# Kernel optimization log

Hardware: AMD Instinct MI355X
Metric: run time of the kernel (lower is better)

Reference implementation:

```python
import jax, jax.numpy as jnp
import numpy as np

B, S, D, H = 2, 2048, 1024, 16
DK = D // H


def setup_inputs() -> dict:
    key = jax.random.key(0)
    ks = jax.random.split(key, 12)
    scale = 1.0 / np.sqrt(D)
    inp = {
        "Q": jax.random.normal(ks[0], (B, S, D), jnp.float32),
        "K": jax.random.normal(ks[1], (B, S, D), jnp.float32),
        "V": jax.random.normal(ks[2], (B, S, D), jnp.float32),
        # causal mask, broadcastable to [B, H, S, S]; 0 -> masked
        "Mask": jnp.tril(jnp.ones((S, S), jnp.int32))[None, None],
        "Wq": jax.random.normal(ks[3], (D, D), jnp.float32) * scale,
        "bq": jnp.zeros((D,), jnp.float32),
        "Wk": jax.random.normal(ks[4], (D, D), jnp.float32) * scale,
        "bk": jnp.zeros((D,), jnp.float32),
        "Wv": jax.random.normal(ks[5], (D, D), jnp.float32) * scale,
        "bv": jnp.zeros((D,), jnp.float32),
        "Wo": jax.random.normal(ks[6], (D, D), jnp.float32) * scale,
        "bo": jnp.zeros((D,), jnp.float32),
    }
    return inp


def _heads(x):
    # [B, S, D] -> [B, H, S, DK]
    return x.reshape(B, S, H, DK).transpose(0, 2, 1, 3)


def reference(Q, K, V, Mask, Wq, bq, Wk, bk, Wv, bv, Wo, bo):
    q = _heads(Q @ Wq.T + bq)
    k = _heads(K @ Wk.T + bk)
    v = _heads(V @ Wv.T + bv)
    # NOTE: original module does NOT scale by 1/sqrt(d_k)
    logits = jnp.einsum("bhqd,bhkd->bhqk", q, k)
    logits = jnp.where(Mask == 0, jnp.float32(-1e9), logits)
    attn = jax.nn.softmax(logits, axis=-1)  # dropout p=0.0 -> identity
    ctx = jnp.einsum("bhqk,bhkd->bhqd", attn, v)
    ctx = ctx.transpose(0, 2, 1, 3).reshape(B, S, D)
    return ctx @ Wo.T + bo
```

## Files before the change

kernel.cpp:

```cpp
#include <hip/hip_runtime.h>
#include <hip/hip_bf16.h>

#define B_  2
#define S_  2048
#define D_  1024
#define H_  16
#define DK_ 64
#define M_  (B_ * S_)

typedef __bf16 bf16;
typedef __bf16 bf16x8 __attribute__((ext_vector_type(8)));
typedef __bf16 bf16x4 __attribute__((ext_vector_type(4)));
typedef float  f32x4  __attribute__((ext_vector_type(4)));

#define MFMA16(a, b, c) __builtin_amdgcn_mfma_f32_16x16x32_bf16((a), (b), (c), 0, 0, 0)

__device__ __forceinline__ void gl2lds16(const bf16* g, bf16* l) {
    __builtin_amdgcn_global_load_lds((const __attribute__((address_space(1))) void*)g,
                                     (__attribute__((address_space(3))) void*)l, 16, 0, 0);
}

struct CastArgs { const float* src[7]; bf16* dst[7]; };

__global__ __launch_bounds__(256) void cast_all(CastArgs a) {
    int i = blockIdx.x * 256 + threadIdx.x;
    int seg, off;
    if (i < 3145728) { seg = i >> 20; off = i & 1048575; }
    else { int j = i - 3145728; seg = 3 + (j >> 18); off = j & 262143; }
    float4 v = ((const float4*)a.src[seg])[off];
    bf16x4 o;
    o[0] = (bf16)v.x; o[1] = (bf16)v.y; o[2] = (bf16)v.z; o[3] = (bf16)v.w;
    *(bf16x4*)&a.dst[seg][(size_t)off * 4] = o;
}

struct QkvArgs { const bf16* A[3]; const bf16* W[3]; const float* bias[3]; bf16* out[3]; };

__global__ __launch_bounds__(256, 3) void gemm_qkv(QkvArgs ar) {
    __shared__ char smem[34816];
    bf16* As = (bf16*)smem;
    bf16* Bs = (bf16*)(smem + 16384);
    bf16* Cs = (bf16*)smem;

    const int z = blockIdx.z;
    const bf16* A  = ar.A[z];
    const bf16* Bt = ar.W[z];
    const float* bias = ar.bias[z];
    bf16* Out = ar.out[z];
    const int mode = (z == 2) ? 1 : 0;

    const int t = threadIdx.x, lane = t & 63, w = t >> 6;
    const int lr = lane & 15, lq = lane >> 4;
    const int wm = (w >> 1) * 64, wn = (w & 1) * 64;
    const int n0 = blockIdx.x * 128, m0 = blockIdx.y * 128;

    const bf16* Ag[4]; const bf16* Bg[4]; bf16* Al[4]; bf16* Bl[4];
#pragma unroll
    for (int i = 0; i < 4; ++i) {
        int c = i * 256 + w * 64 + lane;
        int row = c >> 3, x = (c & 7) ^ (row & 7);
        Ag[i] = A  + (size_t)(m0 + row) * 1024 + x * 8;
        Bg[i] = Bt + (size_t)(n0 + row) * 1024 + x * 8;
        Al[i] = As + (i * 256 + w * 64) * 8;
        Bl[i] = Bs + (i * 256 + w * 64) * 8;
    }

    f32x4 acc[4][4];
#pragma unroll
    for (int mi = 0; mi < 4; ++mi)
#pragma unroll
        for (int ni = 0; ni < 4; ++ni) acc[mi][ni] = 0.0f;

    for (int k0 = 0; k0 < 1024; k0 += 64) {
        __syncthreads();
#pragma unroll
        for (int i = 0; i < 4; ++i) {
            gl2lds16(Ag[i] + k0, Al[i]);
            gl2lds16(Bg[i] + k0, Bl[i]);
        }
        __syncthreads();
#pragma unroll
        for (int ks = 0; ks < 2; ++ks) {
            bf16x8 af[4], bfr[4];
#pragma unroll
            for (int mi = 0; mi < 4; ++mi) {
                int row = wm + mi * 16 + lr;
                af[mi] = *(const bf16x8*)&As[row * 64 + ((ks * 4 + lq) ^ (row & 7)) * 8];
            }
#pragma unroll
            for (int ni = 0; ni < 4; ++ni) {
                int row = wn + ni * 16 + lr;
                bfr[ni] = *(const bf16x8*)&Bs[row * 64 + ((ks * 4 + lq) ^ (row & 7)) * 8];
            }
#pragma unroll
            for (int mi = 0; mi < 4; ++mi)
#pragma unroll
                for (int ni = 0; ni < 4; ++ni) acc[mi][ni] = MFMA16(af[mi], bfr[ni], acc[mi][ni]);
        }
    }

    if (mode == 0) {
#pragma unroll
        for (int mi = 0; mi < 4; ++mi) {
#pragma unroll
            for (int ni = 0; ni < 4; ++ni) {
                int gn = n0 + wn + ni * 16 + lr;
                float bv = bias[gn];
#pragma unroll
                for (int r = 0; r < 4; ++r) {
                    int gm = m0 + wm + mi * 16 + lq * 4 + r;
                    float v = acc[mi][ni][r] + bv;
                    int b = gm >> 11, s = gm & (S_ - 1);
                    int h = gn >> 6, dk = gn & 63;
                    Out[(((size_t)(b * H_ + h) * S_ + s) << 6) + dk] = (bf16)v;
                }
            }
        }
    } else {
        __syncthreads();
#pragma unroll
        for (int mi = 0; mi < 4; ++mi) {
#pragma unroll
            for (int ni = 0; ni < 4; ++ni) {
                int n = wn + ni * 16 + lr;
                float bv = bias[n0 + n];
                bf16x4 pk;
#pragma unroll
                for (int r = 0; r < 4; ++r) pk[r] = (bf16)(acc[mi][ni][r] + bv);
                *(bf16x4*)&Cs[n * 136 + wm + mi * 16 + lq * 4] = pk;
            }
        }
        __syncthreads();
        const int b = m0 >> 11, s0 = m0 & (S_ - 1);
#pragma unroll
        for (int j = 0; j < 8; ++j) {
            int cc = j * 256 + t;
            int n = cc >> 4, cm = cc & 15;
            int gn = n0 + n, h = gn >> 6, dk = gn & 63;
            bf16x8 v = *(const bf16x8*)&Cs[n * 136 + cm * 8];
            *(bf16x8*)&Out[(((size_t)(b * H_ + h) * DK_ + dk) << 11) + s0 + cm * 8] = v;
        }
    }
}

__global__ __launch_bounds__(256, 2) void gemm_out(const bf16* __restrict__ A,
                                                   const bf16* __restrict__ Bt,
                                                   const float* __restrict__ bias,
                                                   float* __restrict__ Out) {
    __shared__ bf16 As[64 * 64];
    __shared__ bf16 Bs[128 * 64];

    const int t = threadIdx.x, lane = t & 63, w = t >> 6;
    const int lr = lane & 15, lq = lane >> 4;
    const int wm = (w >> 1) * 32, wn = (w & 1) * 64;
    const int n0 = blockIdx.x * 128, m0 = blockIdx.y * 64;

    const bf16* Ag[2]; bf16* Al[2];
#pragma unroll
    for (int i = 0; i < 2; ++i) {
        int c = i * 256 + w * 64 + lane;
        int row = c >> 3, x = (c & 7) ^ (row & 7);
        Ag[i] = A + (size_t)(m0 + row) * 1024 + x * 8;
        Al[i] = As + (i * 256 + w * 64) * 8;
    }
    const bf16* Bg[4]; bf16* Bl[4];
#pragma unroll
    for (int i = 0; i < 4; ++i) {
        int c = i * 256 + w * 64 + lane;
        int row = c >> 3, x = (c & 7) ^ (row & 7);
        Bg[i] = Bt + (size_t)(n0 + row) * 1024 + x * 8;
        Bl[i] = Bs + (i * 256 + w * 64) * 8;
    }

    f32x4 acc[2][4];
#pragma unroll
    for (int mi = 0; mi < 2; ++mi)
#pragma unroll
        for (int ni = 0; ni < 4; ++ni) acc[mi][ni] = 0.0f;

    for (int k0 = 0; k0 < 1024; k0 += 64) {
        __syncthreads();
#pragma unroll
        for (int i = 0; i < 2; ++i) gl2lds16(Ag[i] + k0, Al[i]);
#pragma unroll
        for (int i = 0; i < 4; ++i) gl2lds16(Bg[i] + k0, Bl[i]);
        __syncthreads();
#pragma unroll
        for (int ks = 0; ks < 2; ++ks) {
            bf16x8 af[2], bfr[4];
#pragma unroll
            for (int mi = 0; mi < 2; ++mi) {
                int row = wm + mi * 16 + lr;
                af[mi] = *(const bf16x8*)&As[row * 64 + ((ks * 4 + lq) ^ (row & 7)) * 8];
            }
#pragma unroll
            for (int ni = 0; ni < 4; ++ni) {
                int row = wn + ni * 16 + lr;
                bfr[ni] = *(const bf16x8*)&Bs[row * 64 + ((ks * 4 + lq) ^ (row & 7)) * 8];
            }
#pragma unroll
            for (int mi = 0; mi < 2; ++mi)
#pragma unroll
                for (int ni = 0; ni < 4; ++ni) acc[mi][ni] = MFMA16(af[mi], bfr[ni], acc[mi][ni]);
        }
    }

#pragma unroll
    for (int mi = 0; mi < 2; ++mi) {
#pragma unroll
        for (int ni = 0; ni < 4; ++ni) {
            int gn = n0 + wn + ni * 16 + lr;
            float bv = bias[gn];
#pragma unroll
            for (int r = 0; r < 4; ++r) {
                int gm = m0 + wm + mi * 16 + lq * 4 + r;
                Out[(size_t)gm * 1024 + gn] = acc[mi][ni][r] + bv;
            }
        }
    }
}

__global__ __launch_bounds__(256, 2) void flash_attn(const bf16* __restrict__ qh,
                                                     const bf16* __restrict__ kh,
                                                     const bf16* __restrict__ vt,
                                                     bf16* __restrict__ ctx) {
    __shared__ char smem[40960];
    bf16* Qs = (bf16*)smem;
    bf16* Ks = (bf16*)(smem + 8192);
    bf16* Ps = (bf16*)(smem + 24576);

    const int id = blockIdx.x;
    const int xcd = id & 7, loc = id >> 3;
    const int bh = xcd * 4 + (loc & 3);
    const int pair = loc >> 2;
    const int b = bh >> 4, h = bh & 15;

    const bf16* Qp = qh + (size_t)bh * S_ * DK_;
    const bf16* Kp = kh + (size_t)bh * S_ * DK_;
    const bf16* Vp = vt + (size_t)bh * DK_ * S_;

    const int t = threadIdx.x, lane = t & 63, w = t >> 6;
    const int lr = lane & 15, lq = lane >> 4;
    const int wq = w & 1, wk = w >> 1;
    bf16* Pw = Ps + w * 2048;

    for (int half = 0; half < 2; ++half) {
        const int qt = half ? (31 - pair) : pair;

#pragma unroll
        for (int i = 0; i < 2; ++i) {
            int c = w * 128 + i * 64 + lane;
            int qrow = c >> 3, xx = (c & 7) ^ (qrow & 7);
            gl2lds16(Qp + (size_t)(qt * 64 + qrow) * 64 + xx * 8, Qs + (w * 128 + i * 64) * 8);
        }

        f32x4 oacc[2][4];
#pragma unroll
        for (int mt = 0; mt < 2; ++mt)
#pragma unroll
            for (int nt = 0; nt < 4; ++nt) oacc[mt][nt] = 0.0f;
        float lpart[2] = {0.f, 0.f};

        const int nkt = qt / 2 + 1;
        for (int kt = 0; kt < nkt; ++kt) {
            __syncthreads();
#pragma unroll
            for (int i = 0; i < 4; ++i) {
                int c = w * 256 + i * 64 + lane;
                int krow = c >> 3, xx = (c & 7) ^ (krow & 7);
                gl2lds16(Kp + (size_t)(kt * 128 + krow) * 64 + xx * 8, Ks + (w * 256 + i * 64) * 8);
            }
            __syncthreads();

            const int k64 = kt * 2 + wk;
            if (k64 <= qt) {
                bf16x8 bv[2][4];
#pragma unroll
                for (int kk = 0; kk < 2; ++kk)
#pragma unroll
                    for (int nt = 0; nt < 4; ++nt)
                        bv[kk][nt] = *(const bf16x8*)(Vp + (size_t)(nt * 16 + lr) * S_ +
                                                      kt * 128 + wk * 64 + kk * 32 + lq * 8);
                f32x4 s[4][2];
#pragma unroll
                for (int mt = 0; mt < 4; ++mt)
#pragma unroll
                    for (int nt = 0; nt < 2; ++nt) s[mt][nt] = 0.0f;
#pragma unroll
                for (int ks = 0; ks < 2; ++ks) {
                    bf16x8 af[4], qf[2];
                    int xx = (ks * 4 + lq) ^ (lr & 7);
#pragma unroll
                    for (int mt = 0; mt < 4; ++mt)
                        af[mt] = *(const bf16x8*)&Ks[(wk * 64 + mt * 16 + lr) * 64 + xx * 8];
#pragma unroll
                    for (int nt = 0; nt < 2; ++nt)
                        qf[nt] = *(const bf16x8*)&Qs[(wq * 32 + nt * 16 + lr) * 64 + xx * 8];
#pragma unroll
                    for (int mt = 0; mt < 4; ++mt)
#pragma unroll
                        for (int nt = 0; nt < 2; ++nt) s[mt][nt] = MFMA16(af[mt], qf[nt], s[mt][nt]);
                }
                const bool diag = (k64 == qt);
#pragma unroll
                for (int mt = 0; mt < 4; ++mt)
#pragma unroll
                    for (int nt = 0; nt < 2; ++nt) {
                        bf16x4 pb;
#pragma unroll
                        for (int r = 0; r < 4; ++r) {
                            int kl = mt * 16 + lq * 4 + r;
                            int qlT = wq * 32 + nt * 16 + lr;
                            float p = (!diag || kl <= qlT) ? __expf(s[mt][nt][r]) : 0.0f;
                            bf16 p16 = (bf16)p;
                            lpart[nt] += (float)p16;
                            pb[r] = p16;
                        }
                        int xx = (2 * mt + (lq >> 1)) ^ (lr & 7);
                        *(bf16x4*)&Pw[(nt * 16 + lr) * 64 + xx * 8 + (lq & 1) * 4] = pb;
                    }
#pragma unroll
                for (int kk = 0; kk < 2; ++kk) {
                    bf16x8 ap[2];
                    int xx = (kk * 4 + lq) ^ (lr & 7);
#pragma unroll
                    for (int mt2 = 0; mt2 < 2; ++mt2)
                        ap[mt2] = *(const bf16x8*)&Pw[(mt2 * 16 + lr) * 64 + xx * 8];
#pragma unroll
                    for (int mt2 = 0; mt2 < 2; ++mt2)
#pragma unroll
                        for (int nt = 0; nt < 4; ++nt)
                            oacc[mt2][nt] = MFMA16(ap[mt2], bv[kk][nt], oacc[mt2][nt]);
                }
            }
        }

        __syncthreads();
#pragma unroll
        for (int nt = 0; nt < 2; ++nt) {
            lpart[nt] += __shfl_xor(lpart[nt], 16);
            lpart[nt] += __shfl_xor(lpart[nt], 32);
        }
        float* Op = (float*)(smem + 24576);
        float* Lh = (float*)smem;
        if (lq == 0)
#pragma unroll
            for (int nt = 0; nt < 2; ++nt) Lh[wk * 64 + wq * 32 + nt * 16 + lr] = lpart[nt];
        if (wk == 1) {
#pragma unroll
            for (int mt = 0; mt < 2; ++mt)
#pragma unroll
                for (int nt = 0; nt < 4; ++nt)
#pragma unroll
                    for (int r = 0; r < 4; ++r) {
                        int row = mt * 16 + lq * 4 + r, col = nt * 16 + lr;
                        int xx = (col >> 2) ^ (row & 15);
                        Op[wq * 2048 + row * 64 + xx * 4 + (col & 3)] = oacc[mt][nt][r];
                    }
        }
        __syncthreads();
        if (wk == 0) {
            float linv[2][4];
#pragma unroll
            for (int mt = 0; mt < 2; ++mt)
#pragma unroll
                for (int r = 0; r < 4; ++r) {
                    int qq = wq * 32 + mt * 16 + lq * 4 + r;
                    linv[mt][r] = 1.0f / (Lh[qq] + Lh[64 + qq]);
                }
#pragma unroll
            for (int mt = 0; mt < 2; ++mt)
#pragma unroll
                for (int nt = 0; nt < 4; ++nt)
#pragma unroll
                    for (int r = 0; r < 4; ++r) {
                        int row = mt * 16 + lq * 4 + r, col = nt * 16 + lr;
                        int xx = (col >> 2) ^ (row & 15);
                        float v = (oacc[mt][nt][r] + Op[wq * 2048 + row * 64 + xx * 4 + (col & 3)]) * linv[mt][r];
                        int q = qt * 64 + wq * 32 + row;
                        ctx[((size_t)(b * S_ + q)) * D_ + h * DK_ + col] = (bf16)v;
                    }
        }
        __syncthreads();
    }
}

extern "C" void kernel_launch(void* const* d_in, const int* in_sizes, int n_in,
                              void* d_out, int out_size, void* d_ws, size_t ws_size,
                              hipStream_t stream) {
    const float* Q  = (const float*)d_in[0];
    const float* K  = (const float*)d_in[1];
    const float* V  = (const float*)d_in[2];
    const float* Wq = (const float*)d_in[4];
    const float* bq = (const float*)d_in[5];
    const float* Wk = (const float*)d_in[6];
    const float* bk = (const float*)d_in[7];
    const float* Wv = (const float*)d_in[8];
    const float* bv = (const float*)d_in[9];
    const float* Wo = (const float*)d_in[10];
    const float* bo = (const float*)d_in[11];

    char* p = (char*)d_ws;
    bf16* Qb  = (bf16*)p;  p += (size_t)M_ * D_ * 2;
    bf16* Kb  = (bf16*)p;  p += (size_t)M_ * D_ * 2;
    bf16* Vb  = (bf16*)p;  p += (size_t)M_ * D_ * 2;
    bf16* Wqb = (bf16*)p;  p += (size_t)D_ * D_ * 2;
    bf16* Wkb = (bf16*)p;  p += (size_t)D_ * D_ * 2;
    bf16* Wvb = (bf16*)p;  p += (size_t)D_ * D_ * 2;
    bf16* Wob = (bf16*)p;  p += (size_t)D_ * D_ * 2;
    bf16* qhd = (bf16*)p;  p += (size_t)M_ * D_ * 2;
    bf16* khd = (bf16*)p;  p += (size_t)M_ * D_ * 2;
    bf16* vtr = (bf16*)p;  p += (size_t)M_ * D_ * 2;
    bf16* ctx = (bf16*)p;  p += (size_t)M_ * D_ * 2;

    CastArgs ca;
    ca.src[0] = Q;  ca.dst[0] = Qb;
    ca.src[1] = K;  ca.dst[1] = Kb;
    ca.src[2] = V;  ca.dst[2] = Vb;
    ca.src[3] = Wq; ca.dst[3] = Wqb;
    ca.src[4] = Wk; ca.dst[4] = Wkb;
    ca.src[5] = Wv; ca.dst[5] = Wvb;
    ca.src[6] = Wo; ca.dst[6] = Wob;
    cast_all<<<16384, 256, 0, stream>>>(ca);

    QkvArgs qa;
    qa.A[0] = Qb;  qa.A[1] = Kb;  qa.A[2] = Vb;
    qa.W[0] = Wqb; qa.W[1] = Wkb; qa.W[2] = Wvb;
    qa.bias[0] = bq; qa.bias[1] = bk; qa.bias[2] = bv;
    qa.out[0] = qhd; qa.out[1] = khd; qa.out[2] = vtr;
    dim3 qgrid(D_ / 128, M_ / 128, 3);
    gemm_qkv<<<qgrid, 256, 0, stream>>>(qa);

    flash_attn<<<512, 256, 0, stream>>>(qhd, khd, vtr, ctx);

    dim3 ogrid(D_ / 128, M_ / 64);
    gemm_out<<<ogrid, 256, 0, stream>>>(ctx, Wob, bo, (float*)d_out);
}
```

Measured before the change: 228.9 us.

## Split flash attention into one q-tile per block, load K/Q directly to registers

The attention kernel now launches one block per 64-row query tile (1024 blocks) instead of pairing a light and a heavy causal tile in one block. The heaviest tiles get the lowest block ids. Q fragments are held in registers, and K fragments are read straight from global memory instead of being staged through LDS with barriers. This cuts LDS use (17KB vs 40KB) and removes the per-iteration syncthreads. In exchange, K tiles are no longer shared through LDS, so each wave re-reads K from global or L2, and the load balance between blocks becomes uneven.

Result: slower. 255.9 us (+11.8%).

```diff
diff --git a/kernel.cpp b/kernel.cpp
--- a/kernel.cpp
+++ b/kernel.cpp
@@ -223,15 +223,15 @@
                                                      const bf16* __restrict__ kh,
                                                      const bf16* __restrict__ vt,
                                                      bf16* __restrict__ ctx) {
-    __shared__ char smem[40960];
-    bf16* Qs = (bf16*)smem;
-    bf16* Ks = (bf16*)(smem + 8192);
-    bf16* Ps = (bf16*)(smem + 24576);
+    __shared__ char smem[17408];
+    float* Lh = (float*)smem;
+    bf16* Ps = (bf16*)(smem + 1024);
+    float* Op = (float*)(smem + 1024);
 
     const int id = blockIdx.x;
     const int xcd = id & 7, loc = id >> 3;
     const int bh = xcd * 4 + (loc & 3);
-    const int pair = loc >> 2;
+    const int qt = 31 - (loc >> 2);
     const int b = bh >> 4, h = bh & 15;
 
     const bf16* Qp = qh + (size_t)bh * S_ * DK_;
@@ -243,144 +243,128 @@
     const int wq = w & 1, wk = w >> 1;
     bf16* Pw = Ps + w * 2048;
 
-    for (int half = 0; half < 2; ++half) {
-        const int qt = half ? (31 - pair) : pair;
-
-#pragma unroll
-        for (int i = 0; i < 2; ++i) {
-            int c = w * 128 + i * 64 + lane;
-            int qrow = c >> 3, xx = (c & 7) ^ (qrow & 7);
-            gl2lds16(Qp + (size_t)(qt * 64 + qrow) * 64 + xx * 8, Qs + (w * 128 + i * 64) * 8);
-        }
-
-        f32x4 oacc[2][4];
+    bf16x8 qreg[2][2];
+#pragma unroll
+    for (int ks = 0; ks < 2; ++ks)
+#pragma unroll
+        for (int nt = 0; nt < 2; ++nt)
+            qreg[ks][nt] = *(const bf16x8*)(Qp +
+                (size_t)(qt * 64 + wq * 32 + nt * 16 + lr) * 64 + ks * 32 + lq * 8);
+
+    f32x4 oacc[2][4];
+#pragma unroll
+    for (int mt = 0; mt < 2; ++mt)
+#pragma unroll
+        for (int nt = 0; nt < 4; ++nt) oacc[mt][nt] = 0.0f;
+    float lpart[2] = {0.f, 0.f};
+
+    const bf16* Kw = Kp + (size_t)(wk * 64 + lr) * 64 + lq * 8;
+    const bf16* Vw = Vp + (size_t)lr * S_ + wk * 64 + lq * 8;
+
+    const int nkt = qt / 2 + 1;
+    for (int kt = 0; kt < nkt; ++kt) {
+        const int k64 = kt * 2 + wk;
+        if (k64 <= qt) {
+            bf16x8 bv[2][4];
+#pragma unroll
+            for (int kk = 0; kk < 2; ++kk)
+#pragma unroll
+                for (int nt = 0; nt < 4; ++nt)
+                    bv[kk][nt] = *(const bf16x8*)(Vw + (size_t)nt * 16 * S_ +
+                                                  kt * 128 + kk * 32);
+            f32x4 s[4][2];
+#pragma unroll
+            for (int mt = 0; mt < 4; ++mt)
+#pragma unroll
+                for (int nt = 0; nt < 2; ++nt) s[mt][nt] = 0.0f;
+#pragma unroll
+            for (int ks = 0; ks < 2; ++ks) {
+                bf16x8 af[4];
+#pragma unroll
+                for (int mt = 0; mt < 4; ++mt)
+                    af[mt] = *(const bf16x8*)(Kw + (size_t)(kt * 128 + mt * 16) * 64 + ks * 32);
+#pragma unroll
+                for (int mt = 0; mt < 4; ++mt)
+#pragma unroll
+                    for (int nt = 0; nt < 2; ++nt) s[mt][nt] = MFMA16(af[mt], qreg[ks][nt], s[mt][nt]);
+            }
+            const bool diag = (k64 == qt);
+#pragma unroll
+            for (int mt = 0; mt < 4; ++mt)
+#pragma unroll
+                for (int nt = 0; nt < 2; ++nt) {
+                    bf16x4 pb;
+#pragma unroll
+                    for (int r = 0; r < 4; ++r) {
+                        int kl = mt * 16 + lq * 4 + r;
+                        int qlT = wq * 32 + nt * 16 + lr;
+                        float p = (!diag || kl <= qlT) ? __expf(s[mt][nt][r]) : 0.0f;
+                        bf16 p16 = (bf16)p;
+                        lpart[nt] += (float)p16;
+                        pb[r] = p16;
+                    }
+                    int xx = (2 * mt + (lq >> 1)) ^ (lr & 7);
+                    *(bf16x4*)&Pw[(nt * 16 + lr) * 64 + xx * 8 + (lq & 1) * 4] = pb;
+                }
+#pragma unroll
+            for (int kk = 0; kk < 2; ++kk) {
+                bf16x8 ap[2];
+                int xx = (kk * 4 + lq) ^ (lr & 7);
+#pragma unroll
+                for (int mt2 = 0; mt2 < 2; ++mt2)
+                    ap[mt2] = *(const bf16x8*)&Pw[(mt2 * 16 + lr) * 64 + xx * 8];
+#pragma unroll
+                for (int mt2 = 0; mt2 < 2; ++mt2)
+#pragma unroll
+                    for (int nt = 0; nt < 4; ++nt)
+                        oacc[mt2][nt] = MFMA16(ap[mt2], bv[kk][nt], oacc[mt2][nt]);
+            }
+        }
+    }
+
+    __syncthreads();
+#pragma unroll
+    for (int nt = 0; nt < 2; ++nt) {
+        lpart[nt] += __shfl_xor(lpart[nt], 16);
+        lpart[nt] += __shfl_xor(lpart[nt], 32);
+    }
+    if (lq == 0)
+#pragma unroll
+        for (int nt = 0; nt < 2; ++nt) Lh[wk * 64 + wq * 32 + nt * 16 + lr] = lpart[nt];
+    if (wk == 1) {
 #pragma unroll
         for (int mt = 0; mt < 2; ++mt)
 #pragma unroll
-            for (int nt = 0; nt < 4; ++nt) oacc[mt][nt] = 0.0f;
-        float lpart[2] = {0.f, 0.f};
-
-        const int nkt = qt / 2 + 1;
-        for (int kt = 0; kt < nkt; ++kt) {
-            __syncthreads();
-#pragma unroll
-            for (int i = 0; i < 4; ++i) {
-                int c = w * 256 + i * 64 + lane;
-                int krow = c >> 3, xx = (c & 7) ^ (krow & 7);
-                gl2lds16(Kp + (size_t)(kt * 128 + krow) * 64 + xx * 8, Ks + (w * 256 + i * 64) * 8);
-            }
-            __syncthreads();
-
-            const int k64 = kt * 2 + wk;
-            if (k64 <= qt) {
-                bf16x8 bv[2][4];
-#pragma unroll
-                for (int kk = 0; kk < 2; ++kk)
-#pragma unroll
-                    for (int nt = 0; nt < 4; ++nt)
-                        bv[kk][nt] = *(const bf16x8*)(Vp + (size_t)(nt * 16 + lr) * S_ +
-                                                      kt * 128 + wk * 64 + kk * 32 + lq * 8);
-                f32x4 s[4][2];
-#pragma unroll
-                for (int mt = 0; mt < 4; ++mt)
-#pragma unroll
-                    for (int nt = 0; nt < 2; ++nt) s[mt][nt] = 0.0f;
-#pragma unroll
-                for (int ks = 0; ks < 2; ++ks) {
-                    bf16x8 af[4], qf[2];
-                    int xx = (ks * 4 + lq) ^ (lr & 7);
-#pragma unroll
-                    for (int mt = 0; mt < 4; ++mt)
-                        af[mt] = *(const bf16x8*)&Ks[(wk * 64 + mt * 16 + lr) * 64 + xx * 8];
-#pragma unroll
-                    for (int nt = 0; nt < 2; ++nt)
-                        qf[nt] = *(const bf16x8*)&Qs[(wq * 32 + nt * 16 + lr) * 64 + xx * 8];
-#pragma unroll
-                    for (int mt = 0; mt < 4; ++mt)
-#pragma unroll
-                        for (int nt = 0; nt < 2; ++nt) s[mt][nt] = MFMA16(af[mt], qf[nt], s[mt][nt]);
+            for (int nt = 0; nt < 4; ++nt)
+#pragma unroll
+                for (int r = 0; r < 4; ++r) {
+                    int row = mt * 16 + lq * 4 + r, col = nt * 16 + lr;
+                    int xx = (col >> 2) ^ (row & 15);
+                    Op[wq * 2048 + row * 64 + xx * 4 + (col & 3)] = oacc[mt][nt][r];
                 }
-                const bool diag = (k64 == qt);
-#pragma unroll
-                for (int mt = 0; mt < 4; ++mt)
-#pragma unroll
-                    for (int nt = 0; nt < 2; ++nt) {
-                        bf16x4 pb;
-#pragma unroll
-                        for (int r = 0; r < 4; ++r) {
-                            int kl = mt * 16 + lq * 4 + r;
-                            int qlT = wq * 32 + nt * 16 + lr;
-                            float p = (!diag || kl <= qlT) ? __expf(s[mt][nt][r]) : 0.0f;
-                            bf16 p16 = (bf16)p;
-                            lpart[nt] += (float)p16;
-                            pb[r] = p16;
-                        }
-                        int xx = (2 * mt + (lq >> 1)) ^ (lr & 7);
-                        *(bf16x4*)&Pw[(nt * 16 + lr) * 64 + xx * 8 + (lq & 1) * 4] = pb;
-                    }
-#pragma unroll
-                for (int kk = 0; kk < 2; ++kk) {
-                    bf16x8 ap[2];
-                    int xx = (kk * 4 + lq) ^ (lr & 7);
-#pragma unroll
-                    for (int mt2 = 0; mt2 < 2; ++mt2)
-                        ap[mt2] = *(const bf16x8*)&Pw[(mt2 * 16 + lr) * 64 + xx * 8];
-#pragma unroll
-                    for (int mt2 = 0; mt2 < 2; ++mt2)
-#pragma unroll
-                        for (int nt = 0; nt < 4; ++nt)
-                            oacc[mt2][nt] = MFMA16(ap[mt2], bv[kk][nt], oacc[mt2][nt]);
+    }
+    __syncthreads();
+    if (wk == 0) {
+        float linv[2][4];
+#pragma unroll
+        for (int mt = 0; mt < 2; ++mt)
+#pragma unroll
+            for (int r = 0; r < 4; ++r) {
+                int qq = wq * 32 + mt * 16 + lq * 4 + r;
+                linv[mt][r] = 1.0f / (Lh[qq] + Lh[64 + qq]);
+            }
+#pragma unroll
+        for (int mt = 0; mt < 2; ++mt)
+#pragma unroll
+            for (int nt = 0; nt < 4; ++nt)
+#pragma unroll
+                for (int r = 0; r < 4; ++r) {
+                    int row = mt * 16 + lq * 4 + r, col = nt * 16 + lr;
+                    int xx = (col >> 2) ^ (row & 15);
+                    float v = (oacc[mt][nt][r] + Op[wq * 2048 + row * 64 + xx * 4 + (col & 3)]) * linv[mt][r];
+                    int q = qt * 64 + wq * 32 + row;
+                    ctx[((size_t)(b * S_ + q)) * D_ + h * DK_ + col] = (bf16)v;
                 }
-            }
-        }
-
-        __syncthreads();
-#pragma unroll
-        for (int nt = 0; nt < 2; ++nt) {
-            lpart[nt] += __shfl_xor(lpart[nt], 16);
-            lpart[nt] += __shfl_xor(lpart[nt], 32);
-        }
-        float* Op = (float*)(smem + 24576);
-        float* Lh = (float*)smem;
-        if (lq == 0)
-#pragma unroll
-            for (int nt = 0; nt < 2; ++nt) Lh[wk * 64 + wq * 32 + nt * 16 + lr] = lpart[nt];
-        if (wk == 1) {
-#pragma unroll
-            for (int mt = 0; mt < 2; ++mt)
-#pragma unroll
-                for (int nt = 0; nt < 4; ++nt)
-#pragma unroll
-                    for (int r = 0; r < 4; ++r) {
-                        int row = mt * 16 + lq * 4 + r, col = nt * 16 + lr;
-                        int xx = (col >> 2) ^ (row & 15);
-                        Op[wq * 2048 + row * 64 + xx * 4 + (col & 3)] = oacc[mt][nt][r];
-                    }
-        }
-        __syncthreads();
-        if (wk == 0) {
-            float linv[2][4];
-#pragma unroll
-            for (int mt = 0; mt < 2; ++mt)
-#pragma unroll
-                for (int r = 0; r < 4; ++r) {
-                    int qq = wq * 32 + mt * 16 + lq * 4 + r;
-                    linv[mt][r] = 1.0f / (Lh[qq] + Lh[64 + qq]);
-                }
-#pragma unroll
-            for (int mt = 0; mt < 2; ++mt)
-#pragma unroll
-                for (int nt = 0; nt < 4; ++nt)
-#pragma unroll
-                    for (int r = 0; r < 4; ++r) {
-                        int row = mt * 16 + lq * 4 + r, col = nt * 16 + lr;
-                        int xx = (col >> 2) ^ (row & 15);
-                        float v = (oacc[mt][nt][r] + Op[wq * 2048 + row * 64 + xx * 4 + (col & 3)]) * linv[mt][r];
-                        int q = qt * 64 + wq * 32 + row;
-                        ctx[((size_t)(b * S_ + q)) * D_ + h * DK_ + col] = (bf16)v;
-                    }
-        }
-        __syncthreads();
     }
 }
 
@@ -430,7 +414,7 @@
     dim3 qgrid(D_ / 128, M_ / 128, 3);
     gemm_qkv<<<qgrid, 256, 0, stream>>>(qa);
 
-    flash_attn<<<512, 256, 0, stream>>>(qhd, khd, vtr, ctx);
+    flash_attn<<<1024, 256, 0, stream>>>(qhd, khd, vtr, ctx);
 
     dim3 ogrid(D_ / 128, M_ / 64);
     gemm_out<<<ogrid, 256, 0, stream>>>(ctx, Wob, bo, (float*)d_out);
```

## Swizzle GEMM block order across XCDs and keep Q fragments in registers

Applied to the files above, without the earlier changes.

Both GEMM kernels now remap the linear block id so consecutive blocks on the same XCD work on neighbouring tiles, which should improve L2 reuse of the A and W tiles. The flash attention kernel loads its Q fragments directly from global memory into registers once per query tile, instead of staging them in LDS and re-reading them on every key tile. This removes the Q LDS buffer and the repeated LDS reads, and shrinks shared memory. The cost is more register pressure and uncoalesced per-lane global loads for Q.

After: 213.8 us. -6.6%, faster.

```diff
diff --git a/kernel.cpp b/kernel.cpp
--- a/kernel.cpp
+++ b/kernel.cpp
@@ -41,7 +41,10 @@
     bf16* Bs = (bf16*)(smem + 16384);
     bf16* Cs = (bf16*)smem;
 
-    const int z = blockIdx.z;
+    const int hid = (blockIdx.z * gridDim.y + blockIdx.y) * gridDim.x + blockIdx.x;
+    const int swz = (hid & 7) * 96 + (hid >> 3);
+    const int bx = swz & 7, by = (swz >> 3) & 31, z = swz >> 8;
+
     const bf16* A  = ar.A[z];
     const bf16* Bt = ar.W[z];
     const float* bias = ar.bias[z];
@@ -51,7 +54,7 @@
     const int t = threadIdx.x, lane = t & 63, w = t >> 6;
     const int lr = lane & 15, lq = lane >> 4;
     const int wm = (w >> 1) * 64, wn = (w & 1) * 64;
-    const int n0 = blockIdx.x * 128, m0 = blockIdx.y * 128;
+    const int n0 = bx * 128, m0 = by * 128;
 
     const bf16* Ag[4]; const bf16* Bg[4]; bf16* Al[4]; bf16* Bl[4];
 #pragma unroll
@@ -149,10 +152,14 @@
     __shared__ bf16 As[64 * 64];
     __shared__ bf16 Bs[128 * 64];
 
+    const int hid = blockIdx.y * gridDim.x + blockIdx.x;
+    const int swz = (hid & 7) * 64 + (hid >> 3);
+    const int bx = swz & 7, by = swz >> 3;
+
     const int t = threadIdx.x, lane = t & 63, w = t >> 6;
     const int lr = lane & 15, lq = lane >> 4;
     const int wm = (w >> 1) * 32, wn = (w & 1) * 64;
-    const int n0 = blockIdx.x * 128, m0 = blockIdx.y * 64;
+    const int n0 = bx * 128, m0 = by * 64;
 
     const bf16* Ag[2]; bf16* Al[2];
 #pragma unroll
@@ -223,10 +230,11 @@
                                                      const bf16* __restrict__ kh,
                                                      const bf16* __restrict__ vt,
                                                      bf16* __restrict__ ctx) {
-    __shared__ char smem[40960];
-    bf16* Qs = (bf16*)smem;
-    bf16* Ks = (bf16*)(smem + 8192);
-    bf16* Ps = (bf16*)(smem + 24576);
+    __shared__ char smem[33280];
+    bf16* Ks = (bf16*)smem;
+    bf16* Ps = (bf16*)(smem + 16384);
+    float* Op = (float*)(smem + 16384);
+    float* Lh = (float*)(smem + 32768);
 
     const int id = blockIdx.x;
     const int xcd = id & 7, loc = id >> 3;
@@ -246,12 +254,13 @@
     for (int half = 0; half < 2; ++half) {
         const int qt = half ? (31 - pair) : pair;
 
-#pragma unroll
-        for (int i = 0; i < 2; ++i) {
-            int c = w * 128 + i * 64 + lane;
-            int qrow = c >> 3, xx = (c & 7) ^ (qrow & 7);
-            gl2lds16(Qp + (size_t)(qt * 64 + qrow) * 64 + xx * 8, Qs + (w * 128 + i * 64) * 8);
-        }
+        bf16x8 qreg[2][2];
+#pragma unroll
+        for (int ks = 0; ks < 2; ++ks)
+#pragma unroll
+            for (int nt = 0; nt < 2; ++nt)
+                qreg[ks][nt] = *(const bf16x8*)(Qp +
+                    (size_t)(qt * 64 + wq * 32 + nt * 16 + lr) * 64 + ks * 32 + lq * 8);
 
         f32x4 oacc[2][4];
 #pragma unroll
@@ -287,18 +296,15 @@
                     for (int nt = 0; nt < 2; ++nt) s[mt][nt] = 0.0f;
 #pragma unroll
                 for (int ks = 0; ks < 2; ++ks) {
-                    bf16x8 af[4], qf[2];
+                    bf16x8 af[4];
                     int xx = (ks * 4 + lq) ^ (lr & 7);
 #pragma unroll
                     for (int mt = 0; mt < 4; ++mt)
                         af[mt] = *(const bf16x8*)&Ks[(wk * 64 + mt * 16 + lr) * 64 + xx * 8];
 #pragma unroll
-                    for (int nt = 0; nt < 2; ++nt)
-                        qf[nt] = *(const bf16x8*)&Qs[(wq * 32 + nt * 16 + lr) * 64 + xx * 8];
-#pragma unroll
                     for (int mt = 0; mt < 4; ++mt)
 #pragma unroll
-                        for (int nt = 0; nt < 2; ++nt) s[mt][nt] = MFMA16(af[mt], qf[nt], s[mt][nt]);
+                        for (int nt = 0; nt < 2; ++nt) s[mt][nt] = MFMA16(af[mt], qreg[ks][nt], s[mt][nt]);
                 }
                 const bool diag = (k64 == qt);
 #pragma unroll
@@ -340,8 +346,6 @@
             lpart[nt] += __shfl_xor(lpart[nt], 16);
             lpart[nt] += __shfl_xor(lpart[nt], 32);
         }
-        float* Op = (float*)(smem + 24576);
-        float* Lh = (float*)smem;
         if (lq == 0)
 #pragma unroll
             for (int nt = 0; nt < 2; ++nt) Lh[wk * 64 + wq * 32 + nt * 16 + lr] = lpart[nt];
```
